# Kernel tuning notes

Hardware: AMD Instinct MI355X
Metric: run time of the kernel (lower is better)

## Reference

```python
import jax, jax.numpy as jnp
import numpy as np

H = 512          # hidden_size
B = 1024         # batch
T = 256          # warmup sequence length
NUM_STEPS = 64


def setup_inputs() -> dict:
    key = jax.random.key(0)
    ks = jax.random.split(key, 8)
    bound = 1.0 / np.sqrt(H)  # torch default init for RNN/Linear
    x = jax.random.normal(ks[0], (B, T), dtype=jnp.float32)
    W_ih = jax.random.uniform(ks[1], (H, 1), jnp.float32, -bound, bound)
    W_hh = jax.random.uniform(ks[2], (H, H), jnp.float32, -bound, bound)
    b_ih = jax.random.uniform(ks[3], (H,), jnp.float32, -bound, bound)
    b_hh = jax.random.uniform(ks[4], (H,), jnp.float32, -bound, bound)
    W_fc = jax.random.uniform(ks[5], (1, H), jnp.float32, -bound, bound)
    b_fc = jax.random.uniform(ks[6], (1,), jnp.float32, -bound, bound)
    return {"x": x, "W_ih": W_ih, "W_hh": W_hh, "b_ih": b_ih,
            "b_hh": b_hh, "W_fc": W_fc, "b_fc": b_fc, "num_steps": NUM_STEPS}


def reference(x, W_ih, W_hh, b_ih, b_hh, W_fc, b_fc, num_steps):
    # Phase 1: warmup RNN over the input series. h_t = relu(x_t*W_ih + b_ih + h@W_hh^T + b_hh)
    bias = b_ih + b_hh  # [H]
    w_in = W_ih[:, 0]   # [H], input_size == 1

    def warm_step(h, xt):                      # h: [B,H], xt: [B]
        h = jax.nn.relu(xt[:, None] * w_in[None, :] + h @ W_hh.T + bias)
        return h, None

    h0 = jnp.zeros((B, H), dtype=x.dtype)
    h, _ = jax.lax.scan(warm_step, h0, x.T)    # scan over time: x.T is [T,B]

    def roll_step(h, _):
        y = h @ W_fc.T + b_fc                  # [B,1]
        h = jax.nn.relu(y @ W_ih.T + h @ W_hh.T + bias)
        return h, y

    _, ys = jax.lax.scan(roll_step, h, None, length=num_steps)  # ys: [S,B,1]
    return jnp.transpose(ys, (1, 0, 2))        # [B, num_steps, 1]
```

## Files before the change

kernel.cpp:

```cpp
#include <hip/hip_runtime.h>
#include <stdint.h>

#define H 512
#define B_SZ 1024
#define T_WARM 256
#define NSTEPS 64
#define TOTAL_T (T_WARM + NSTEPS)

#define RPB 16
#define NTEAM 64
#define NCG 4
#define NBLK 256
#define NTHR 512

#define ROWB 1024

typedef __attribute__((ext_vector_type(8))) short bf16x8;
typedef __attribute__((ext_vector_type(4))) float f32x4;

static __device__ __forceinline__ ushort f2bf(float f) {
    uint32_t u = __builtin_bit_cast(uint32_t, f);
    u += 0x7FFFu + ((u >> 16) & 1u);
    return (ushort)(u >> 16);
}
static __device__ __forceinline__ float bf2f(ushort h) {
    uint32_t u = ((uint32_t)h) << 16;
    return __builtin_bit_cast(float, u);
}

__global__ void prep_kernel(const float* __restrict__ x,
                            const float* __restrict__ W_hh,
                            const float* __restrict__ b_ih,
                            const float* __restrict__ b_hh,
                            ushort* __restrict__ Wh, ushort* __restrict__ Wl,
                            float* __restrict__ bias, float* __restrict__ xT,
                            uint32_t* __restrict__ Hb0, uint32_t* __restrict__ flags) {
    int i = blockIdx.x * NTHR + threadIdx.x;
    Hb0[i] = 0u;
    if (i < 4096) flags[i] = 0u;
    if (i < H * H) {
        float w = W_hh[i];
        ushort hi = f2bf(w);
        Wh[i] = hi;
        Wl[i] = f2bf(w - bf2f(hi));
    }
    if (i < B_SZ * T_WARM) {
        int b = i & (B_SZ - 1), t = i >> 10;
        xT[t * B_SZ + b] = x[b * T_WARM + t];
    }
    if (i < H) bias[i] = b_ih[i] + b_hh[i];
}

__global__ __launch_bounds__(NTHR, 1)
void rnn_kernel(const float* __restrict__ xT,
                const float* __restrict__ W_ih,
                const float* __restrict__ b_fc_p,
                const float* __restrict__ W_fc,
                const ushort* __restrict__ Wh_g,
                const ushort* __restrict__ Wl_g,
                const float* __restrict__ bias_g,
                uint32_t* __restrict__ Hb0, uint32_t* __restrict__ Hb1,
                uint32_t* __restrict__ flags,
                float* __restrict__ out) {
    __shared__ __align__(16) ushort h_hi[2][RPB * 512];
    __shared__ __align__(16) ushort h_lo[2][RPB * 512];
    __shared__ __align__(16) float  w_fc_s[H];

    const int tid  = threadIdx.x;
    const int bid  = blockIdx.x;
    const int team = bid & (NTEAM - 1);
    const int cg   = bid >> 6;
    const int row0 = team * RPB;
    const int col0 = cg * 128;

    const int lane = tid & 63;
    const int wv   = tid >> 6;
    const int n    = lane & 15, q = lane >> 4;
    const bool selfw = ((wv >> 1) == cg);

    w_fc_s[tid] = W_fc[tid];
    for (int i = tid; i < RPB * 512; i += NTHR) { h_hi[0][i] = 0; h_lo[0][i] = 0; }

    bf16x8 Bh[16], Bl[16];
    {
        const ushort* wh = Wh_g + (col0 + wv * 16 + n) * H + q * 8;
        const ushort* wl = Wl_g + (col0 + wv * 16 + n) * H + q * 8;
        #pragma unroll
        for (int i = 0; i < 16; ++i) {
            const int ktg = (cg * 4 + i) & 15;
            Bh[i] = *(const bf16x8*)(wh + ktg * 32);
            Bl[i] = *(const bf16x8*)(wl + ktg * 32);
        }
    }
    const float wi  = W_ih[col0 + wv * 16 + n];
    const float bj  = bias_g[col0 + wv * 16 + n];
    const float bfc = b_fc_p[0];

    uint32_t* const myflag =
        flags + (((team * NCG + cg) * 2 + (wv >> 2)) << 2) + (wv & 3);
    const uint64_t* const pollp =
        (const uint64_t*)(flags + (((team * NCG + (wv >> 1)) * 2 + (wv & 1)) << 2));

    char* const hb0c = (char*)&h_hi[0][0];
    char* const hb1c = (char*)&h_hi[1][0];
    char* const lb0c = (char*)&h_lo[0][0];
    char* const lb1c = (char*)&h_lo[1][0];

    __syncthreads();

    for (int t = 0; t < TOTAL_T; ++t) {
        const int pp = t & 1;
        const bool roll = (t >= T_WARM);

        f32x4 xq = {0.f, 0.f, 0.f, 0.f};
        if (!roll) xq = *(const f32x4*)(xT + t * B_SZ + row0 + q * 4);

        __syncthreads();

        uint64_t tmp[8];
        const bool stage = (!selfw) && (t > 0);
        if (stage) {
            const uint32_t need = (uint32_t)t;
            while (true) {
                uint64_t f = __hip_atomic_load(pollp, __ATOMIC_RELAXED, __HIP_MEMORY_SCOPE_AGENT);
                if ((uint32_t)f >= need && (uint32_t)(f >> 32) >= need) break;
                __builtin_amdgcn_s_sleep(1);
            }
            const uint64_t* src = (const uint64_t*)((t & 1) ? Hb1 : Hb0);
            #pragma unroll
            for (int it = 0; it < 8; ++it) {
                int idx = it * 64 + lane;
                int r = idx >> 5, c = idx & 31;
                tmp[it] = __hip_atomic_load(src + ((row0 + r) * 256 + wv * 32 + c),
                                            __ATOMIC_RELAXED, __HIP_MEMORY_SCOPE_AGENT);
            }
        }

        const char* ha = pp ? hb1c : hb0c;
        const char* la = pp ? lb1c : lb0c;
        const int aoffs = n * ROWB + q * 16;
        const int aswz  = (n & 3) << 5;
        f32x4 a0 = {0.f, 0.f, 0.f, 0.f}, a1 = {0.f, 0.f, 0.f, 0.f};
        float yp = 0.f;
        #pragma unroll
        for (int kk = 0; kk < 4; ++kk) {
            const int ktg = cg * 4 + kk;
            const int b0 = (aoffs + ktg * 64) ^ aswz;
            bf16x8 ah = *(const bf16x8*)(ha + b0);
            bf16x8 al = *(const bf16x8*)(la + b0);
            f32x4& ac = (kk & 1) ? a1 : a0;
            ac = __builtin_amdgcn_mfma_f32_16x16x32_bf16(ah, Bh[kk], ac, 0, 0, 0);
            ac = __builtin_amdgcn_mfma_f32_16x16x32_bf16(al, Bh[kk], ac, 0, 0, 0);
            ac = __builtin_amdgcn_mfma_f32_16x16x32_bf16(ah, Bl[kk], ac, 0, 0, 0);
            if (roll) {
                const float* wf = &w_fc_s[ktg * 32 + q * 8];
                f32x4 w0 = *(const f32x4*)wf;
                f32x4 w1 = *(const f32x4*)(wf + 4);
                #pragma unroll
                for (int j = 0; j < 4; ++j) {
                    yp += (bf2f((ushort)ah[j])     + bf2f((ushort)al[j]))     * w0[j];
                    yp += (bf2f((ushort)ah[j + 4]) + bf2f((ushort)al[j + 4])) * w1[j];
                }
            }
        }

        if (stage) {
            char* hb = pp ? hb1c : hb0c;
            char* lb = pp ? lb1c : lb0c;
            #pragma unroll
            for (int it = 0; it < 8; ++it) {
                int idx = it * 64 + lane;
                int r = idx >> 5, c = idx & 31;
                int byte = (r * ROWB + wv * 128 + c * 4) ^ ((r & 3) << 5);
                uint64_t u = tmp[it];
                uint32_t w0 = (uint32_t)u, w1 = (uint32_t)(u >> 32);
                *(uint32_t*)(hb + byte) = (w0 >> 16) | (w1 & 0xFFFF0000u);
                *(uint32_t*)(lb + byte) = (w0 & 0xFFFFu) | (w1 << 16);
            }
        }
        __syncthreads();

        #pragma unroll
        for (int i = 4; i < 16; ++i) {
            const int ktg = (cg * 4 + i) & 15;
            const int b0 = (aoffs + ktg * 64) ^ aswz;
            bf16x8 ah = *(const bf16x8*)(ha + b0);
            bf16x8 al = *(const bf16x8*)(la + b0);
            f32x4& ac = (i & 1) ? a1 : a0;
            ac = __builtin_amdgcn_mfma_f32_16x16x32_bf16(ah, Bh[i], ac, 0, 0, 0);
            ac = __builtin_amdgcn_mfma_f32_16x16x32_bf16(al, Bh[i], ac, 0, 0, 0);
            ac = __builtin_amdgcn_mfma_f32_16x16x32_bf16(ah, Bl[i], ac, 0, 0, 0);
            if (roll) {
                const float* wf = &w_fc_s[ktg * 32 + q * 8];
                f32x4 w0 = *(const f32x4*)wf;
                f32x4 w1 = *(const f32x4*)(wf + 4);
                #pragma unroll
                for (int j = 0; j < 4; ++j) {
                    yp += (bf2f((ushort)ah[j])     + bf2f((ushort)al[j]))     * w0[j];
                    yp += (bf2f((ushort)ah[j + 4]) + bf2f((ushort)al[j + 4])) * w1[j];
                }
            }
        }

        float yfin = 0.f;
        if (roll) {
            yp += __shfl_xor(yp, 16);
            yp += __shfl_xor(yp, 32);
            yfin = yp + bfc;
            if (cg == 0 && wv == 0 && lane < 16)
                out[(row0 + lane) * NSTEPS + (t - T_WARM)] = yfin;
        }

        uint32_t* hbn = (t & 1) ? Hb0 : Hb1;
        char* dh = pp ? hb0c : hb1c;
        char* dl = pp ? lb0c : lb1c;
        const int jcol = col0 + wv * 16 + n;
        #pragma unroll
        for (int i = 0; i < 4; ++i) {
            const int m = q * 4 + i;
            const float sv = roll ? __shfl(yfin, m) : xq[i];
            float v = a0[i] + a1[i] + sv * wi + bj;
            v = fmaxf(v, 0.f);
            const ushort hb16 = f2bf(v);
            const ushort lb16 = f2bf(v - bf2f(hb16));
            const uint32_t pk = ((uint32_t)hb16 << 16) | lb16;
            __hip_atomic_store(hbn + (row0 + m) * H + jcol, pk,
                               __ATOMIC_RELAXED, __HIP_MEMORY_SCOPE_AGENT);
            const uint32_t nb = __shfl_xor(pk, 1);
            if ((n & 1) == 0) {
                const int byte = (m * ROWB + jcol * 2) ^ ((m & 3) << 5);
                *(uint32_t*)(dh + byte) = (pk >> 16)     | (nb & 0xFFFF0000u);
                *(uint32_t*)(dl + byte) = (pk & 0xFFFFu) | (nb << 16);
            }
        }
        asm volatile("s_waitcnt vmcnt(0)" ::: "memory");
        if (lane == 0)
            __hip_atomic_store(myflag, (uint32_t)(t + 1),
                               __ATOMIC_RELAXED, __HIP_MEMORY_SCOPE_AGENT);
    }
}

extern "C" void kernel_launch(void* const* d_in, const int* in_sizes, int n_in,
                              void* d_out, int out_size, void* d_ws, size_t ws_size,
                              hipStream_t stream) {
    const float* x    = (const float*)d_in[0];
    const float* W_ih = (const float*)d_in[1];
    const float* W_hh = (const float*)d_in[2];
    const float* b_ih = (const float*)d_in[3];
    const float* b_hh = (const float*)d_in[4];
    const float* W_fc = (const float*)d_in[5];
    const float* b_fc = (const float*)d_in[6];
    float* out = (float*)d_out;

    uint8_t* w = (uint8_t*)d_ws;
    ushort*   Wh    = (ushort*)(w);
    ushort*   Wl    = (ushort*)(w + 524288);
    float*    bias  = (float*)(w + 1048576);
    float*    xT    = (float*)(w + 1052672);
    uint32_t* Hb0   = (uint32_t*)(w + 2101248);
    uint32_t* Hb1   = (uint32_t*)(w + 4198400);
    uint32_t* flags = (uint32_t*)(w + 6295552);

    prep_kernel<<<1024, NTHR, 0, stream>>>(x, W_hh, b_ih, b_hh, Wh, Wl, bias, xT, Hb0, flags);
    rnn_kernel<<<NBLK, NTHR, 0, stream>>>(xT, W_ih, b_fc, W_fc, Wh, Wl, bias, Hb0, Hb1, flags, out);
}
```

Before: 1.205 ms.

## Fold output projection into recurrent weights and split hi/lo exchange buffers

During rollout the feedback y·W_ih term is folded into W_hh by adding the outer product W_ih·W_fc (and b_fc·W_ih into the bias) once at the warmup boundary. This removes the per-step dot product and shuffle that made each new state wait on y, and saves one loop iteration. y is now built from per-column partial products of the new h, reduced by atomicAdd into an accumulator, with a separate kernel adding b_fc. The global exchange buffers are split into hi/lo planes written as packed pairs, so staging becomes plain 64-bit copies. The first __syncthreads is moved after the loads and the LDS swizzle is changed. The folded weights are re-rounded to bf16 hi/lo, and the float atomics make the sum order nondeterministic, so results may differ slightly.

```diff
diff --git a/kernel.cpp b/kernel.cpp
--- a/kernel.cpp
+++ b/kernel.cpp
@@ -5,14 +5,13 @@
 #define B_SZ 1024
 #define T_WARM 256
 #define NSTEPS 64
-#define TOTAL_T (T_WARM + NSTEPS)
+#define TLOOP (T_WARM + NSTEPS - 1)
 
 #define RPB 16
 #define NTEAM 64
 #define NCG 4
 #define NBLK 256
 #define NTHR 512
-
 #define ROWB 1024
 
 typedef __attribute__((ext_vector_type(8))) short bf16x8;
@@ -34,21 +33,30 @@
                             const float* __restrict__ b_hh,
                             ushort* __restrict__ Wh, ushort* __restrict__ Wl,
                             float* __restrict__ bias, float* __restrict__ xT,
-                            uint32_t* __restrict__ Hb0, uint32_t* __restrict__ flags) {
+                            uint32_t* __restrict__ HbH0, uint32_t* __restrict__ HbL0,
+                            float* __restrict__ Yacc, uint32_t* __restrict__ flags) {
     int i = blockIdx.x * NTHR + threadIdx.x;
-    Hb0[i] = 0u;
+    HbH0[i] = 0u; HbL0[i] = 0u;
     if (i < 4096) flags[i] = 0u;
-    if (i < H * H) {
+    if (i < B_SZ * NSTEPS) Yacc[i] = 0.f;
+    {
         float w = W_hh[i];
         ushort hi = f2bf(w);
         Wh[i] = hi;
         Wl[i] = f2bf(w - bf2f(hi));
     }
-    if (i < B_SZ * T_WARM) {
+    {
         int b = i & (B_SZ - 1), t = i >> 10;
         xT[t * B_SZ + b] = x[b * T_WARM + t];
     }
     if (i < H) bias[i] = b_ih[i] + b_hh[i];
+}
+
+__global__ void fix_kernel(const float* __restrict__ Yacc,
+                           const float* __restrict__ b_fc_p,
+                           float* __restrict__ out) {
+    int i = blockIdx.x * 256 + threadIdx.x;
+    out[i] = Yacc[i] + b_fc_p[0];
 }
 
 __global__ __launch_bounds__(NTHR, 1)
@@ -59,9 +67,10 @@
                 const ushort* __restrict__ Wh_g,
                 const ushort* __restrict__ Wl_g,
                 const float* __restrict__ bias_g,
-                uint32_t* __restrict__ Hb0, uint32_t* __restrict__ Hb1,
-                uint32_t* __restrict__ flags,
-                float* __restrict__ out) {
+                uint32_t* __restrict__ HbH0, uint32_t* __restrict__ HbH1,
+                uint32_t* __restrict__ HbL0, uint32_t* __restrict__ HbL1,
+                float* __restrict__ Yacc,
+                uint32_t* __restrict__ flags) {
     __shared__ __align__(16) ushort h_hi[2][RPB * 512];
     __shared__ __align__(16) ushort h_lo[2][RPB * 512];
     __shared__ __align__(16) float  w_fc_s[H];
@@ -92,8 +101,10 @@
             Bl[i] = *(const bf16x8*)(wl + ktg * 32);
         }
     }
-    const float wi  = W_ih[col0 + wv * 16 + n];
-    const float bj  = bias_g[col0 + wv * 16 + n];
+    const int jcol  = col0 + wv * 16 + n;
+    const float wi  = W_ih[jcol];
+    const float wfcj = W_fc[jcol];
+    float bj = bias_g[jcol];
     const float bfc = b_fc_p[0];
 
     uint32_t* const myflag =
@@ -108,16 +119,33 @@
 
     __syncthreads();
 
-    for (int t = 0; t < TOTAL_T; ++t) {
+    for (int t = 0; t < TLOOP; ++t) {
         const int pp = t & 1;
         const bool roll = (t >= T_WARM);
 
+        if (t == T_WARM) {
+            #pragma unroll
+            for (int i = 0; i < 16; ++i) {
+                const int ktg = (cg * 4 + i) & 15;
+                const float* wf = &w_fc_s[ktg * 32 + q * 8];
+                f32x4 w0 = *(const f32x4*)wf;
+                f32x4 w1 = *(const f32x4*)(wf + 4);
+                #pragma unroll
+                for (int j = 0; j < 8; ++j) {
+                    const float wk = (j < 4) ? w0[j] : w1[j - 4];
+                    float v = bf2f((ushort)Bh[i][j]) + bf2f((ushort)Bl[i][j]) + wi * wk;
+                    const ushort hb16 = f2bf(v);
+                    Bh[i][j] = (short)hb16;
+                    Bl[i][j] = (short)f2bf(v - bf2f(hb16));
+                }
+            }
+            bj += bfc * wi;
+        }
+
         f32x4 xq = {0.f, 0.f, 0.f, 0.f};
         if (!roll) xq = *(const f32x4*)(xT + t * B_SZ + row0 + q * 4);
 
-        __syncthreads();
-
-        uint64_t tmp[8];
+        uint64_t tmpH[4], tmpL[4];
         const bool stage = (!selfw) && (t > 0);
         if (stage) {
             const uint32_t need = (uint32_t)t;
@@ -126,22 +154,25 @@
                 if ((uint32_t)f >= need && (uint32_t)(f >> 32) >= need) break;
                 __builtin_amdgcn_s_sleep(1);
             }
-            const uint64_t* src = (const uint64_t*)((t & 1) ? Hb1 : Hb0);
-            #pragma unroll
-            for (int it = 0; it < 8; ++it) {
+            const uint64_t* sH = (const uint64_t*)(pp ? HbH1 : HbH0);
+            const uint64_t* sL = (const uint64_t*)(pp ? HbL1 : HbL0);
+            #pragma unroll
+            for (int it = 0; it < 4; ++it) {
                 int idx = it * 64 + lane;
-                int r = idx >> 5, c = idx & 31;
-                tmp[it] = __hip_atomic_load(src + ((row0 + r) * 256 + wv * 32 + c),
-                                            __ATOMIC_RELAXED, __HIP_MEMORY_SCOPE_AGENT);
-            }
-        }
+                int r = idx >> 4, u = idx & 15;
+                size_t off = (size_t)(row0 + r) * 128 + wv * 16 + u;
+                tmpH[it] = __hip_atomic_load(sH + off, __ATOMIC_RELAXED, __HIP_MEMORY_SCOPE_AGENT);
+                tmpL[it] = __hip_atomic_load(sL + off, __ATOMIC_RELAXED, __HIP_MEMORY_SCOPE_AGENT);
+            }
+        }
+
+        __syncthreads();
 
         const char* ha = pp ? hb1c : hb0c;
         const char* la = pp ? lb1c : lb0c;
         const int aoffs = n * ROWB + q * 16;
-        const int aswz  = (n & 3) << 5;
+        const int aswz  = (n & 7) << 4;
         f32x4 a0 = {0.f, 0.f, 0.f, 0.f}, a1 = {0.f, 0.f, 0.f, 0.f};
-        float yp = 0.f;
         #pragma unroll
         for (int kk = 0; kk < 4; ++kk) {
             const int ktg = cg * 4 + kk;
@@ -152,30 +183,18 @@
             ac = __builtin_amdgcn_mfma_f32_16x16x32_bf16(ah, Bh[kk], ac, 0, 0, 0);
             ac = __builtin_amdgcn_mfma_f32_16x16x32_bf16(al, Bh[kk], ac, 0, 0, 0);
             ac = __builtin_amdgcn_mfma_f32_16x16x32_bf16(ah, Bl[kk], ac, 0, 0, 0);
-            if (roll) {
-                const float* wf = &w_fc_s[ktg * 32 + q * 8];
-                f32x4 w0 = *(const f32x4*)wf;
-                f32x4 w1 = *(const f32x4*)(wf + 4);
-                #pragma unroll
-                for (int j = 0; j < 4; ++j) {
-                    yp += (bf2f((ushort)ah[j])     + bf2f((ushort)al[j]))     * w0[j];
-                    yp += (bf2f((ushort)ah[j + 4]) + bf2f((ushort)al[j + 4])) * w1[j];
-                }
-            }
         }
 
         if (stage) {
             char* hb = pp ? hb1c : hb0c;
             char* lb = pp ? lb1c : lb0c;
             #pragma unroll
-            for (int it = 0; it < 8; ++it) {
+            for (int it = 0; it < 4; ++it) {
                 int idx = it * 64 + lane;
-                int r = idx >> 5, c = idx & 31;
-                int byte = (r * ROWB + wv * 128 + c * 4) ^ ((r & 3) << 5);
-                uint64_t u = tmp[it];
-                uint32_t w0 = (uint32_t)u, w1 = (uint32_t)(u >> 32);
-                *(uint32_t*)(hb + byte) = (w0 >> 16) | (w1 & 0xFFFF0000u);
-                *(uint32_t*)(lb + byte) = (w0 & 0xFFFFu) | (w1 << 16);
+                int r = idx >> 4, u = idx & 15;
+                int byte = (r * ROWB + wv * 128 + u * 8) ^ ((r & 7) << 4);
+                *(uint64_t*)(hb + byte) = tmpH[it];
+                *(uint64_t*)(lb + byte) = tmpL[it];
             }
         }
         __syncthreads();
@@ -190,53 +209,57 @@
             ac = __builtin_amdgcn_mfma_f32_16x16x32_bf16(ah, Bh[i], ac, 0, 0, 0);
             ac = __builtin_amdgcn_mfma_f32_16x16x32_bf16(al, Bh[i], ac, 0, 0, 0);
             ac = __builtin_amdgcn_mfma_f32_16x16x32_bf16(ah, Bl[i], ac, 0, 0, 0);
-            if (roll) {
-                const float* wf = &w_fc_s[ktg * 32 + q * 8];
-                f32x4 w0 = *(const f32x4*)wf;
-                f32x4 w1 = *(const f32x4*)(wf + 4);
-                #pragma unroll
-                for (int j = 0; j < 4; ++j) {
-                    yp += (bf2f((ushort)ah[j])     + bf2f((ushort)al[j]))     * w0[j];
-                    yp += (bf2f((ushort)ah[j + 4]) + bf2f((ushort)al[j + 4])) * w1[j];
-                }
-            }
-        }
-
-        float yfin = 0.f;
-        if (roll) {
-            yp += __shfl_xor(yp, 16);
-            yp += __shfl_xor(yp, 32);
-            yfin = yp + bfc;
-            if (cg == 0 && wv == 0 && lane < 16)
-                out[(row0 + lane) * NSTEPS + (t - T_WARM)] = yfin;
-        }
-
-        uint32_t* hbn = (t & 1) ? Hb0 : Hb1;
+        }
+
+        uint32_t* dH = pp ? HbH0 : HbH1;
+        uint32_t* dL = pp ? HbL0 : HbL1;
         char* dh = pp ? hb0c : hb1c;
         char* dl = pp ? lb0c : lb1c;
-        const int jcol = col0 + wv * 16 + n;
+        const int colp2 = (col0 + wv * 16 + (n & ~1)) * 2;
+        const size_t gcol = (size_t)((col0 + wv * 16) >> 1) + (n >> 1);
+        const bool capy = (t >= T_WARM - 1);
+        float sarr[4];
         #pragma unroll
         for (int i = 0; i < 4; ++i) {
             const int m = q * 4 + i;
-            const float sv = roll ? __shfl(yfin, m) : xq[i];
-            float v = a0[i] + a1[i] + sv * wi + bj;
+            float v = a0[i] + a1[i] + bj;
+            if (!roll) v += xq[i] * wi;
             v = fmaxf(v, 0.f);
+            sarr[i] = v * wfcj;
             const ushort hb16 = f2bf(v);
             const ushort lb16 = f2bf(v - bf2f(hb16));
             const uint32_t pk = ((uint32_t)hb16 << 16) | lb16;
-            __hip_atomic_store(hbn + (row0 + m) * H + jcol, pk,
-                               __ATOMIC_RELAXED, __HIP_MEMORY_SCOPE_AGENT);
             const uint32_t nb = __shfl_xor(pk, 1);
-            if ((n & 1) == 0) {
-                const int byte = (m * ROWB + jcol * 2) ^ ((m & 3) << 5);
-                *(uint32_t*)(dh + byte) = (pk >> 16)     | (nb & 0xFFFF0000u);
-                *(uint32_t*)(dl + byte) = (pk & 0xFFFFu) | (nb << 16);
-            }
-        }
+            uint32_t pw;
+            if ((n & 1) == 0) pw = (pk >> 16) | (nb & 0xFFFF0000u);
+            else              pw = (nb & 0xFFFFu) | (pk << 16);
+            uint32_t* gdst = ((n & 1) ? dL : dH) + (size_t)(row0 + m) * 256 + gcol;
+            __hip_atomic_store(gdst, pw, __ATOMIC_RELAXED, __HIP_MEMORY_SCOPE_AGENT);
+            const int sbyte = (m * ROWB + colp2) ^ ((m & 7) << 4);
+            *(uint32_t*)(((n & 1) ? dl : dh) + sbyte) = pw;
+        }
+
+        if (capy) {
+            #pragma unroll
+            for (int i = 0; i < 4; ++i) {
+                float s = sarr[i];
+                s += __shfl_xor(s, 1); s += __shfl_xor(s, 2);
+                s += __shfl_xor(s, 4); s += __shfl_xor(s, 8);
+                sarr[i] = s;
+            }
+        }
+
         asm volatile("s_waitcnt vmcnt(0)" ::: "memory");
         if (lane == 0)
             __hip_atomic_store(myflag, (uint32_t)(t + 1),
                                __ATOMIC_RELAXED, __HIP_MEMORY_SCOPE_AGENT);
+
+        if (capy && n == 0) {
+            #pragma unroll
+            for (int i = 0; i < 4; ++i)
+                atomicAdd(Yacc + (size_t)(row0 + q * 4 + i) * NSTEPS + (t + 1 - T_WARM),
+                          sarr[i]);
+        }
     }
 }
 
@@ -257,10 +280,16 @@
     ushort*   Wl    = (ushort*)(w + 524288);
     float*    bias  = (float*)(w + 1048576);
     float*    xT    = (float*)(w + 1052672);
-    uint32_t* Hb0   = (uint32_t*)(w + 2101248);
-    uint32_t* Hb1   = (uint32_t*)(w + 4198400);
-    uint32_t* flags = (uint32_t*)(w + 6295552);
-
-    prep_kernel<<<1024, NTHR, 0, stream>>>(x, W_hh, b_ih, b_hh, Wh, Wl, bias, xT, Hb0, flags);
-    rnn_kernel<<<NBLK, NTHR, 0, stream>>>(xT, W_ih, b_fc, W_fc, Wh, Wl, bias, Hb0, Hb1, flags, out);
-}
+    uint32_t* HbH0  = (uint32_t*)(w + 2101248);
+    uint32_t* HbH1  = (uint32_t*)(w + 3149824);
+    uint32_t* HbL0  = (uint32_t*)(w + 4198400);
+    uint32_t* HbL1  = (uint32_t*)(w + 5246976);
+    float*    Yacc  = (float*)(w + 6295552);
+    uint32_t* flags = (uint32_t*)(w + 6557696);
+
+    prep_kernel<<<512, NTHR, 0, stream>>>(x, W_hh, b_ih, b_hh, Wh, Wl, bias, xT,
+                                          HbH0, HbL0, Yacc, flags);
+    rnn_kernel<<<NBLK, NTHR, 0, stream>>>(xT, W_ih, b_fc, W_fc, Wh, Wl, bias,
+                                          HbH0, HbH1, HbL0, HbL1, Yacc, flags);
+    fix_kernel<<<256, 256, 0, stream>>>(Yacc, b_fc, out);
+}
```

New measurement: 1.382 ms. 1.15x slower.
